# Kernel optimization log

Hardware: AMD Instinct MI355X
Metric: run time of the kernel (lower is better)

The kernel has to match this reference:

```python
import math
import jax, jax.numpy as jnp
import numpy as np

D_MODEL = 1024
N_HEAD = 16
HEAD_DIM = D_MODEL // N_HEAD
ATTN_MULT = 1.0
# standparam=False (muP): scaling = head_dim**-1 * sqrt(attn_mult)
SCALING = (1.0 / HEAD_DIM) * math.sqrt(ATTN_MULT)
EPS = 1e-5


def layernorm(x, w, b):
    mu = jnp.mean(x, axis=-1, keepdims=True)
    var = jnp.mean(jnp.square(x - mu), axis=-1, keepdims=True)
    return (x - mu) * jax.lax.rsqrt(var + EPS) * w + b


def setup_inputs() -> dict:
    key = jax.random.key(0)
    ks = jax.random.split(key, 6)
    L, N, E = 2048, 2, D_MODEL
    std = 0.02
    return {
        "x": jax.random.normal(ks[0], (L, N, E), jnp.float32),
        "ln1_w": jnp.ones((E,), jnp.float32),
        "ln1_b": jnp.zeros((E,), jnp.float32),
        "in_proj_w": jax.random.normal(ks[1], (3 * E, E), jnp.float32) * std,
        "in_proj_b": jnp.zeros((3 * E,), jnp.float32),
        "out_w": jax.random.normal(ks[2], (E, E), jnp.float32) * std,
        "out_b": jnp.zeros((E,), jnp.float32),
        "ln2_w": jnp.ones((E,), jnp.float32),
        "ln2_b": jnp.zeros((E,), jnp.float32),
        "fc_w": jax.random.normal(ks[3], (4 * E, E), jnp.float32) * std,
        "fc_b": jnp.zeros((4 * E,), jnp.float32),
        "proj_w": jax.random.normal(ks[4], (E, 4 * E), jnp.float32) * std,
        "proj_b": jnp.zeros((E,), jnp.float32),
    }


def block(x, ln1_w, ln1_b, in_proj_w, in_proj_b, out_w, out_b,
          ln2_w, ln2_b, fc_w, fc_b, proj_w, proj_b):
    L, N, E = x.shape
    H, D = N_HEAD, HEAD_DIM
    # --- self-attention on ln_1(x), seq-first layout (L, N, E) ---
    y = layernorm(x, ln1_w, ln1_b)
    qkv = jnp.einsum('lne,fe->lnf', y, in_proj_w) + in_proj_b  # (L, N, 3E)
    q, k, v = jnp.split(qkv, 3, axis=-1)
    q = q * SCALING
    # (L, N, E) -> (N, H, L, D)
    def to_heads(t):
        return t.reshape(L, N, H, D).transpose(1, 2, 0, 3)
    q, k, v = to_heads(q), to_heads(k), to_heads(v)
    scores = jnp.einsum('nhld,nhsd->nhls', q, k)           # (N, H, L, L)
    w = jax.nn.softmax(scores, axis=-1)
    o = jnp.einsum('nhls,nhsd->nhld', w, v)                # (N, H, L, D)
    o = o.transpose(2, 0, 1, 3).reshape(L, N, E)
    attn_out = jnp.einsum('lne,fe->lnf', o, out_w) + out_b
    x = x + attn_out
    # --- MLP on ln_2(x): fc -> GELU -> proj ---
    z = layernorm(x, ln2_w, ln2_b)
    h = jax.nn.gelu(jnp.einsum('lne,fe->lnf', z, fc_w) + fc_b, approximate=False)
    m = jnp.einsum('lnf,ef->lne', h, proj_w) + proj_b
    return x + m


def reference(x, ln1_w, ln1_b, in_proj_w, in_proj_b, out_w, out_b,
              ln2_w, ln2_b, fc_w, fc_b, proj_w, proj_b):
    return block(x, ln1_w, ln1_b, in_proj_w, in_proj_b, out_w, out_b,
                 ln2_w, ln2_b, fc_w, fc_b, proj_w, proj_b)
```

## Files before the change

kernel.cpp:

```cpp
#include <hip/hip_runtime.h>
#include <hip/hip_bf16.h>

typedef unsigned short u16;
typedef float v4f __attribute__((ext_vector_type(4)));
typedef __bf16 v8bf __attribute__((ext_vector_type(8)));
typedef unsigned short v4u __attribute__((ext_vector_type(4)));
typedef unsigned short v8u __attribute__((ext_vector_type(8)));

#define EMB 1024
#define TOK 4096
#define LSEQ 2048
#define NBATCH 2
#define SCALING 0.015625f
#define LN_EPS 1e-5f

template <int V> struct ic { static constexpr int v = V; };

__device__ __forceinline__ float bf2f(u16 u) {
  unsigned int i = ((unsigned int)u) << 16;
  return __builtin_bit_cast(float, i);
}
__device__ __forceinline__ u16 f2bf(float f) {
  __hip_bfloat16 h = __float2bfloat16(f);
  return __builtin_bit_cast(u16, h);
}
__device__ __forceinline__ v8bf load8(const u16* p) {
  return *reinterpret_cast<const v8bf*>(p);
}
__device__ __forceinline__ v4f mfma16(v8bf a, v8bf b, v4f c) {
  return __builtin_amdgcn_mfma_f32_16x16x32_bf16(a, b, c, 0, 0, 0);
}
__device__ __forceinline__ void gload16(const u16* g, u16* l) {
  __builtin_amdgcn_global_load_lds(
      (const __attribute__((address_space(1))) void*)g,
      (__attribute__((address_space(3))) void*)l, 16, 0, 0);
}
template <int N>
__device__ __forceinline__ void waitcnt_vm() {
  if constexpr (N == 0) asm volatile("s_waitcnt vmcnt(0)" ::: "memory");
  else if constexpr (N == 2) asm volatile("s_waitcnt vmcnt(2)" ::: "memory");
  else if constexpr (N == 3) asm volatile("s_waitcnt vmcnt(3)" ::: "memory");
  else if constexpr (N == 4) asm volatile("s_waitcnt vmcnt(4)" ::: "memory");
  else if constexpr (N == 6) asm volatile("s_waitcnt vmcnt(6)" ::: "memory");
  else if constexpr (N == 8) asm volatile("s_waitcnt vmcnt(8)" ::: "memory");
}
__device__ __forceinline__ float gelu_fast(float v) {
  float u = v * (0.7978845608f + 0.0356774081f * v * v);
  return v / (1.0f + __expf(-2.0f * u));
}

__global__ __launch_bounds__(256) void cvt_kernel(
    const float* __restrict__ in, u16* __restrict__ out) {
  size_t i = ((size_t)blockIdx.x * 256 + threadIdx.x) * 8;
  v4f a = *reinterpret_cast<const v4f*>(in + i);
  v4f b = *reinterpret_cast<const v4f*>(in + i + 4);
  v8u r;
#pragma unroll
  for (int j = 0; j < 4; j++) { r[j] = f2bf(a[j]); r[4 + j] = f2bf(b[j]); }
  *reinterpret_cast<v8u*>(out + i) = r;
}

__global__ __launch_bounds__(256) void addred_kernel(
    float* __restrict__ out, const u16* __restrict__ p0) {
  size_t i = ((size_t)blockIdx.x * 256 + threadIdx.x) * 8;
  v4f a0 = *reinterpret_cast<const v4f*>(out + i);
  v4f a1 = *reinterpret_cast<const v4f*>(out + i + 4);
  v8u pp = *reinterpret_cast<const v8u*>(p0 + i);
#pragma unroll
  for (int j = 0; j < 4; j++) {
    a0[j] += bf2f(pp[j]);
    a1[j] += bf2f(pp[4 + j]);
  }
  *reinterpret_cast<v4f*>(out + i) = a0;
  *reinterpret_cast<v4f*>(out + i + 4) = a1;
}

template <int MODE>
__global__ __launch_bounds__(256) void ln_kernel(
    const void* __restrict__ xin, const float* __restrict__ w,
    const float* __restrict__ b, u16* __restrict__ y) {
  int t = blockIdx.x, tid = threadIdx.x;
  float v[4];
  if (MODE == 0) {
    v4u raw = *reinterpret_cast<const v4u*>((const u16*)xin + (size_t)t * EMB + tid * 4);
#pragma unroll
    for (int j = 0; j < 4; j++) v[j] = bf2f(raw[j]);
  } else {
    v4f raw = *reinterpret_cast<const v4f*>((const float*)xin + (size_t)t * EMB + tid * 4);
#pragma unroll
    for (int j = 0; j < 4; j++) v[j] = raw[j];
  }
  float s = v[0] + v[1] + v[2] + v[3];
  float ss = v[0] * v[0] + v[1] * v[1] + v[2] * v[2] + v[3] * v[3];
#pragma unroll
  for (int off = 32; off >= 1; off >>= 1) {
    s += __shfl_xor(s, off);
    ss += __shfl_xor(ss, off);
  }
  __shared__ float sm[4], sq[4];
  if ((tid & 63) == 0) { sm[tid >> 6] = s; sq[tid >> 6] = ss; }
  __syncthreads();
  s = sm[0] + sm[1] + sm[2] + sm[3];
  ss = sq[0] + sq[1] + sq[2] + sq[3];
  float mu = s * (1.0f / EMB);
  float var = ss * (1.0f / EMB) - mu * mu;
  float rstd = rsqrtf(var + LN_EPS);
  v4f wv = *reinterpret_cast<const v4f*>(w + tid * 4);
  v4f bv = *reinterpret_cast<const v4f*>(b + tid * 4);
  v4u out;
#pragma unroll
  for (int j = 0; j < 4; j++) out[j] = f2bf((v[j] - mu) * rstd * wv[j] + bv[j]);
  *reinterpret_cast<v4u*>(y + (size_t)t * EMB + tid * 4) = out;
}

template <int BM, int BN>
__global__ __launch_bounds__(256) void gemm_db_kernel(
    const u16* __restrict__ A, const u16* __restrict__ W,
    const float* __restrict__ bias, int K, int Nout, int mode,
    u16* __restrict__ out_bf, float* __restrict__ out_f,
    const float* __restrict__ res_f32, const u16* __restrict__ res_bf) {
  constexpr int NJ = BM * BN / 4096;
  constexpr int CWV = 4 / (BM / 64);
  __shared__ alignas(16) u16 lA[2][BM * 32];
  __shared__ alignas(16) u16 lB[2][BN * 32];

  int tid = threadIdx.x;
  int lane = tid & 63, wid = tid >> 6;
  int quad = lane >> 4, l16 = lane & 15;
  int row0 = blockIdx.x * BM;
  int col0 = blockIdx.y * BN;
  int rw = (wid / CWV) * 64;
  int cw = (wid % CWV) * (BN / CWV);

  v4f zero = {0.f, 0.f, 0.f, 0.f};
  v4f acc[4][NJ];
#pragma unroll
  for (int i = 0; i < 4; i++)
#pragma unroll
    for (int j = 0; j < NJ; j++) acc[i][j] = zero;

  int wbase8 = (tid & 192) * 8;

  auto stage = [&](int buf, int k0) {
    const u16* Ab = A + (size_t)row0 * K + k0;
    const u16* Wb = W + (size_t)col0 * K + k0;
#pragma unroll
    for (int n = 0; n < BM / 64; n++) {
      int slot = n * 256 + tid;
      int seg = slot / BM, r = slot & (BM - 1);
      gload16(Ab + (size_t)r * K + seg * 8, &lA[buf][n * 2048 + wbase8]);
    }
#pragma unroll
    for (int n = 0; n < BN / 64; n++) {
      int slot = n * 256 + tid;
      int seg = slot / BN, r = slot & (BN - 1);
      gload16(Wb + (size_t)r * K + seg * 8, &lB[buf][n * 2048 + wbase8]);
    }
  };

  stage(0, 0);
  int buf = 0;
  for (int k0 = 0; k0 < K; k0 += 32) {
    __syncthreads();
    if (k0 + 32 < K) stage(buf ^ 1, k0 + 32);

    v8bf af[4], bfr[NJ];
#pragma unroll
    for (int i = 0; i < 4; i++)
      af[i] = load8(&lA[buf][(quad * BM + rw + i * 16 + l16) * 8]);
#pragma unroll
    for (int j = 0; j < NJ; j++)
      bfr[j] = load8(&lB[buf][(quad * BN + cw + j * 16 + l16) * 8]);
#pragma unroll
    for (int i = 0; i < 4; i++)
#pragma unroll
      for (int j = 0; j < NJ; j++)
        acc[i][j] = mfma16(af[i], bfr[j], acc[i][j]);
    buf ^= 1;
  }

#pragma unroll
  for (int i = 0; i < 4; i++) {
    int rbase = row0 + rw + i * 16 + quad * 4;
#pragma unroll
    for (int j = 0; j < NJ; j++) {
      int c = col0 + cw + j * 16 + l16;
      float bv = bias[c];
#pragma unroll
      for (int r = 0; r < 4; r++) {
        int tok = rbase + r;
        float v = acc[i][j][r] + bv;
        size_t idx = (size_t)tok * Nout + c;
        if (mode == 1) {
          out_bf[idx] = f2bf(res_f32[idx] + v);
        } else if (mode == 3) {
          out_f[idx] = bf2f(res_bf[idx]) + v;
        }
      }
    }
  }
}

template <int BM, int BN>
__global__ __launch_bounds__(512, 2) void gemm8_kernel(
    const u16* __restrict__ A, const u16* __restrict__ W,
    const float* __restrict__ bias, int K, int Nout, int mode,
    u16* __restrict__ out_bf, float* __restrict__ out_f,
    const u16* __restrict__ res_bf) {
  static_assert(BM == 256 && (BN == 128 || BN == 256), "geometry");
  constexpr int NJF = BN / 128;
  constexpr int LB = BN / 128;
  constexpr int H = BN / 8;
  __shared__ alignas(16) u16 lA[2][2][8192];
  __shared__ alignas(16) u16 lB[2][2][BN * 32];

  int tid = threadIdx.x;
  int lane = tid & 63, wid = tid >> 6;
  int quad = lane >> 4, l16 = lane & 15;
  int rwh = wid >> 2;
  int cwq = wid & 3;
  int row0 = blockIdx.x * BM, col0 = blockIdx.y * BN;

  int kbeg = 0, kend = K;
  if (mode == 5) { int h = K >> 1; kbeg = blockIdx.z * h; kend = kbeg + h; }
  int nt = (kend - kbeg) >> 6;

  v4f zero = {0.f, 0.f, 0.f, 0.f};
  v4f acc[8][2 * NJF];
#pragma unroll
  for (int i = 0; i < 8; i++)
#pragma unroll
    for (int j = 0; j < 2 * NJF; j++) acc[i][j] = zero;

  int wslot = tid & 448;

  auto stA = [&](int buf, int g, int kt) {
    int koff = kbeg + kt * 64;
#pragma unroll
    for (int n = 0; n < 2; n++) {
      int p = n * 512 + tid;
      int ri = p >> 3, sp = p & 7;
      int row = ((ri >> 6) << 7) | (g << 6) | (ri & 63);
      int sl = sp ^ (ri & 7);
      gload16(A + (size_t)(row0 + row) * K + koff + sl * 8,
              &lA[buf][g][(n * 512 + wslot) * 8]);
    }
  };
  auto stB = [&](int buf, int g, int kt) {
    int koff = kbeg + kt * 64;
#pragma unroll
    for (int n = 0; n < LB; n++) {
      int p = n * 512 + tid;
      int ci = p >> 3, sp = p & 7;
      int col = (ci / H) * (2 * H) + g * H + (ci % H);
      int sl = sp ^ (ci & 7);
      gload16(W + (size_t)(col0 + col) * K + koff + sl * 8,
              &lB[buf][g][(n * 512 + wslot) * 8]);
    }
  };

  auto rdA = [&](v8bf (&af)[4][2], int buf, int g) {
#pragma unroll
    for (int i = 0; i < 4; i++) {
      int ri = (rwh << 6) + i * 16 + l16;
      int rs = ri * 8, rx = ri & 7;
#pragma unroll
      for (int kk = 0; kk < 2; kk++)
        af[i][kk] = load8(&lA[buf][g][(rs + ((kk * 4 + quad) ^ rx)) * 8]);
    }
  };
  auto rdB = [&](v8bf (&bf)[NJF][2], int buf, int g) {
#pragma unroll
    for (int j = 0; j < NJF; j++) {
      int ci = cwq * H + j * 16 + l16;
      int rs = ci * 8, rx = ci & 7;
#pragma unroll
      for (int kk = 0; kk < 2; kk++)
        bf[j][kk] = load8(&lB[buf][g][(rs + ((kk * 4 + quad) ^ rx)) * 8]);
    }
  };
  auto mm = [&](auto QA, auto QB, v8bf (&af)[4][2], v8bf (&bf)[NJF][2]) {
    constexpr int qa = decltype(QA)::v, qb = decltype(QB)::v;
#pragma unroll
    for (int i = 0; i < 4; i++)
#pragma unroll
      for (int j = 0; j < NJF; j++)
#pragma unroll
        for (int kk = 0; kk < 2; kk++)
          acc[qa * 4 + i][qb * NJF + j] =
              mfma16(af[i][kk], bf[j][kk], acc[qa * 4 + i][qb * NJF + j]);
  };

  v8bf af[4][2], b0[NJF][2], b1[NJF][2];

  stA(0, 0, 0); stB(0, 0, 0); stB(0, 1, 0); stA(0, 1, 0);
  waitcnt_vm<2 + LB>();
  __builtin_amdgcn_s_barrier();

  for (int t = 0; t < nt - 1; ++t) {
    int buf = t & 1, nb = buf ^ 1;
    rdA(af, buf, 0); rdB(b0, buf, 0);
    stA(nb, 0, t + 1);
    __builtin_amdgcn_s_barrier();
    __builtin_amdgcn_s_setprio(1);
    mm(ic<0>{}, ic<0>{}, af, b0);
    __builtin_amdgcn_s_setprio(0);
    waitcnt_vm<4>();
    __builtin_amdgcn_s_barrier();
    rdB(b1, buf, 1);
    stB(nb, 0, t + 1);
    __builtin_amdgcn_s_barrier();
    __builtin_amdgcn_s_setprio(1);
    mm(ic<0>{}, ic<1>{}, af, b1);
    __builtin_amdgcn_s_setprio(0);
    waitcnt_vm<2 + LB>();
    __builtin_amdgcn_s_barrier();
    rdA(af, buf, 1);
    stB(nb, 1, t + 1);
    __builtin_amdgcn_s_barrier();
    __builtin_amdgcn_s_setprio(1);
    mm(ic<1>{}, ic<1>{}, af, b1);
    __builtin_amdgcn_s_setprio(0);
    __builtin_amdgcn_s_barrier();
    stA(nb, 1, t + 1);
    __builtin_amdgcn_s_barrier();
    __builtin_amdgcn_s_setprio(1);
    mm(ic<1>{}, ic<0>{}, af, b0);
    __builtin_amdgcn_s_setprio(0);
    waitcnt_vm<2 + LB>();
    __builtin_amdgcn_s_barrier();
  }
  waitcnt_vm<0>();
  __builtin_amdgcn_s_barrier();
  {
    int buf = (nt - 1) & 1;
    rdA(af, buf, 0); rdB(b0, buf, 0); rdB(b1, buf, 1);
    mm(ic<0>{}, ic<0>{}, af, b0);
    mm(ic<0>{}, ic<1>{}, af, b1);
    rdA(af, buf, 1);
    mm(ic<1>{}, ic<1>{}, af, b1);
    mm(ic<1>{}, ic<0>{}, af, b0);
  }

  int rw = rwh << 7;
  int cw = cwq * (BN / 4);
#pragma unroll
  for (int i = 0; i < 8; i++) {
    int rbase = row0 + rw + i * 16 + quad * 4;
#pragma unroll
    for (int j = 0; j < 2 * NJF; j++) {
      int c = col0 + cw + j * 16 + l16;
      float bv = bias[c];
#pragma unroll
      for (int r = 0; r < 4; r++) {
        int tok = rbase + r;
        float raw = acc[i][j][r];
        float v = raw + bv;
        if (mode == 4) {
          int region = c >> 10;
          int cc = c & 1023;
          int hh = cc >> 6, dd = cc & 63;
          int l = tok >> 1, nn = tok & 1;
          size_t hb = (size_t)(nn * 16 + hh);
          if (region == 0) {
            out_bf[(hb * LSEQ + l) * 64 + dd] = f2bf(v * SCALING);
          } else if (region == 1) {
            out_bf[4194304 + (hb * LSEQ + l) * 64 + dd] = f2bf(v);
          } else {
            out_bf[8388608 + (hb * 64 + dd) * LSEQ + l] = f2bf(v);
          }
        } else {
          size_t idx = (size_t)tok * Nout + c;
          if (mode == 2) {
            out_bf[idx] = f2bf(gelu_fast(v));
          } else {
            if (blockIdx.z == 0) {
              out_bf[idx] = f2bf(raw);
            } else {
              out_f[idx] = v + bf2f(res_bf[idx]);
            }
          }
        }
      }
    }
  }
}

__global__ __launch_bounds__(512) void flash_kernel(
    const u16* __restrict__ qb, const u16* __restrict__ kb,
    const u16* __restrict__ vtb, u16* __restrict__ o) {
  int tid = threadIdx.x;
  int lane = tid & 63, wid = tid >> 6;
  int quad = lane >> 4, l16 = lane & 15;
  int qt = blockIdx.x;
  int nh = blockIdx.y;
  int n = nh >> 4, h = nh & 15;

  __shared__ alignas(16) u16 lK[4096];
  __shared__ alignas(16) u16 lV[4096];
  __shared__ alignas(16) u16 pl[128][72];

  const u16* khead = kb + (size_t)nh * (LSEQ * 64);
  const u16* vhead = vtb + (size_t)nh * (64 * LSEQ);

  v4f zero = {0.f, 0.f, 0.f, 0.f};
  v4f acc_o[4];
  float lsum[4];
#pragma unroll
  for (int r = 0; r < 4; r++) lsum[r] = 0.f;
#pragma unroll
  for (int jd = 0; jd < 4; jd++) acc_o[jd] = zero;

  v8bf qf[2];
  {
    int lq = qt * 128 + wid * 16 + l16;
#pragma unroll
    for (int kk = 0; kk < 2; kk++)
      qf[kk] = load8(qb + ((size_t)nh * LSEQ + lq) * 64 + kk * 32 + quad * 8);
  }

  int swl = l16 & 7;
  int srow = tid >> 3;
  int sseg0 = tid & 7;
  int lbase = (tid & 448) * 8;

  for (int s0 = 0; s0 < LSEQ; s0 += 64) {
    {
      int seg = sseg0 ^ (srow & 7);
      gload16(khead + (size_t)(s0 + srow) * 64 + seg * 8, &lK[lbase]);
      gload16(vhead + (size_t)srow * LSEQ + s0 + seg * 8, &lV[lbase]);
    }
    __syncthreads();

    v4f sacc[4];
#pragma unroll
    for (int j = 0; j < 4; j++) sacc[j] = zero;
#pragma unroll
    for (int kk = 0; kk < 2; kk++) {
      v8bf kf[4];
#pragma unroll
      for (int j = 0; j < 4; j++) {
        int rl = j * 16 + l16;
        kf[j] = load8(&lK[((rl << 3) + (((kk << 2) + quad) ^ swl)) << 3]);
      }
#pragma unroll
      for (int j = 0; j < 4; j++)
        sacc[j] = mfma16(qf[kk], kf[j], sacc[j]);
    }

#pragma unroll
    for (int r = 0; r < 4; r++) {
      float ps = 0.f;
#pragma unroll
      for (int j = 0; j < 4; j++) {
        float p = __expf(fminf(sacc[j][r], 60.f));
        ps += p;
        pl[wid * 16 + quad * 4 + r][j * 16 + l16] = f2bf(p);
      }
      lsum[r] += ps;
    }

#pragma unroll
    for (int kk = 0; kk < 2; kk++) {
      v8bf pf, vf[4];
      pf = load8(&pl[wid * 16 + l16][kk * 32 + quad * 8]);
#pragma unroll
      for (int jd = 0; jd < 4; jd++) {
        int dl = jd * 16 + l16;
        vf[jd] = load8(&lV[((dl << 3) + (((kk << 2) + quad) ^ swl)) << 3]);
      }
#pragma unroll
      for (int jd = 0; jd < 4; jd++)
        acc_o[jd] = mfma16(pf, vf[jd], acc_o[jd]);
    }
    __syncthreads();
  }

#pragma unroll
  for (int r = 0; r < 4; r++) {
    float s = lsum[r];
#pragma unroll
    for (int off = 1; off < 16; off <<= 1) s += __shfl_xor(s, off);
    float inv = 1.0f / s;
    int lq = qt * 128 + wid * 16 + quad * 4 + r;
    size_t t = (size_t)lq * NBATCH + n;
#pragma unroll
    for (int jd = 0; jd < 4; jd++)
      o[t * EMB + h * 64 + jd * 16 + l16] = f2bf(acc_o[jd][r] * inv);
  }
}

extern "C" void kernel_launch(void* const* d_in, const int* in_sizes, int n_in,
                              void* d_out, int out_size, void* d_ws,
                              size_t ws_size, hipStream_t stream) {
  const float* x = (const float*)d_in[0];
  const float* ln1_w = (const float*)d_in[1];
  const float* ln1_b = (const float*)d_in[2];
  const float* in_proj_w = (const float*)d_in[3];
  const float* in_proj_b = (const float*)d_in[4];
  const float* out_w = (const float*)d_in[5];
  const float* out_b = (const float*)d_in[6];
  const float* ln2_w = (const float*)d_in[7];
  const float* ln2_b = (const float*)d_in[8];
  const float* fc_w = (const float*)d_in[9];
  const float* fc_b = (const float*)d_in[10];
  const float* proj_w = (const float*)d_in[11];
  const float* proj_b = (const float*)d_in[12];
  float* out = (float*)d_out;

  char* ws = (char*)d_ws;
  u16* wbuf = (u16*)(ws + 0);
  u16* y = (u16*)(ws + 8388608);
  u16* qkvh = (u16*)(ws + 16777216);
  u16* o = (u16*)(ws + 8388608);
  u16* hbuf = (u16*)(ws + 8388608);
  u16* x2 = (u16*)(ws + 41943040);
  u16* z = (u16*)(ws + 50331648);

  u16* qb = qkvh;
  u16* kb = qkvh + 4194304;
  u16* vtb = qkvh + 8388608;

  ln_kernel<1><<<TOK, 256, 0, stream>>>((const void*)x, ln1_w, ln1_b, y);
  cvt_kernel<<<1536, 256, 0, stream>>>(in_proj_w, wbuf);
  gemm8_kernel<256, 256><<<dim3(16, 12), 512, 0, stream>>>(
      y, wbuf, in_proj_b, EMB, 3 * EMB, 4, qkvh, nullptr, nullptr);
  flash_kernel<<<dim3(16, 32), 512, 0, stream>>>(qb, kb, vtb, o);
  cvt_kernel<<<512, 256, 0, stream>>>(out_w, wbuf);
  gemm_db_kernel<64, 128><<<dim3(64, 8), 256, 0, stream>>>(
      o, wbuf, out_b, EMB, EMB, 1, x2, nullptr, x, nullptr);
  ln_kernel<0><<<TOK, 256, 0, stream>>>((const void*)x2, ln2_w, ln2_b, z);
  cvt_kernel<<<2048, 256, 0, stream>>>(fc_w, wbuf);
  gemm8_kernel<256, 256><<<dim3(16, 16), 512, 0, stream>>>(
      z, wbuf, fc_b, EMB, 4 * EMB, 2, hbuf, nullptr, nullptr);
  cvt_kernel<<<2048, 256, 0, stream>>>(proj_w, wbuf);
  gemm8_kernel<256, 128><<<dim3(16, 8, 2), 512, 0, stream>>>(
      hbuf, wbuf, proj_b, 4 * EMB, EMB, 5, z, out, x2);
  addred_kernel<<<2048, 256, 0, stream>>>(out, z);
}
```

Before: 419.1 us.

## Swizzle GEMM LDS tiles and double-buffer K/V tiles in flash attention

The GEMM staging now stores A and W tiles in a row-major, XOR-swizzled LDS layout, and the fragment loads use the matching addresses, to reduce LDS bank conflicts. The flash-attention kernel gets double-buffered K and V LDS tiles: the next tile is prefetched with direct global-to-LDS loads and selective vmcnt waits while the current tile is computed, hiding global load latency. This doubles K/V LDS use, which could lower occupancy. It also relies on raw s_barrier placement being correct with respect to the waits.

```diff
diff --git a/kernel.cpp b/kernel.cpp
--- a/kernel.cpp
+++ b/kernel.cpp
@@ -146,15 +146,17 @@
     const u16* Wb = W + (size_t)col0 * K + k0;
 #pragma unroll
     for (int n = 0; n < BM / 64; n++) {
-      int slot = n * 256 + tid;
-      int seg = slot / BM, r = slot & (BM - 1);
-      gload16(Ab + (size_t)r * K + seg * 8, &lA[buf][n * 2048 + wbase8]);
+      int p = n * 256 + tid;
+      int r = p >> 2, sp = p & 3;
+      int sl = sp ^ ((r >> 1) & 3);
+      gload16(Ab + (size_t)r * K + sl * 8, &lA[buf][n * 2048 + wbase8]);
     }
 #pragma unroll
     for (int n = 0; n < BN / 64; n++) {
-      int slot = n * 256 + tid;
-      int seg = slot / BN, r = slot & (BN - 1);
-      gload16(Wb + (size_t)r * K + seg * 8, &lB[buf][n * 2048 + wbase8]);
+      int p = n * 256 + tid;
+      int r = p >> 2, sp = p & 3;
+      int sl = sp ^ ((r >> 1) & 3);
+      gload16(Wb + (size_t)r * K + sl * 8, &lB[buf][n * 2048 + wbase8]);
     }
   };
 
@@ -166,11 +168,15 @@
 
     v8bf af[4], bfr[NJ];
 #pragma unroll
-    for (int i = 0; i < 4; i++)
-      af[i] = load8(&lA[buf][(quad * BM + rw + i * 16 + l16) * 8]);
-#pragma unroll
-    for (int j = 0; j < NJ; j++)
-      bfr[j] = load8(&lB[buf][(quad * BN + cw + j * 16 + l16) * 8]);
+    for (int i = 0; i < 4; i++) {
+      int ra = rw + i * 16 + l16;
+      af[i] = load8(&lA[buf][((ra << 2) + (quad ^ ((ra >> 1) & 3))) << 3]);
+    }
+#pragma unroll
+    for (int j = 0; j < NJ; j++) {
+      int rb = cw + j * 16 + l16;
+      bfr[j] = load8(&lB[buf][((rb << 2) + (quad ^ ((rb >> 1) & 3))) << 3]);
+    }
 #pragma unroll
     for (int i = 0; i < 4; i++)
 #pragma unroll
@@ -396,8 +402,8 @@
   int nh = blockIdx.y;
   int n = nh >> 4, h = nh & 15;
 
-  __shared__ alignas(16) u16 lK[4096];
-  __shared__ alignas(16) u16 lV[4096];
+  __shared__ alignas(16) u16 lK[2][4096];
+  __shared__ alignas(16) u16 lV[2][4096];
   __shared__ alignas(16) u16 pl[128][72];
 
   const u16* khead = kb + (size_t)nh * (LSEQ * 64);
@@ -423,14 +429,23 @@
   int srow = tid >> 3;
   int sseg0 = tid & 7;
   int lbase = (tid & 448) * 8;
-
+  int sseg = sseg0 ^ (srow & 7);
+
+  gload16(khead + (size_t)srow * 64 + sseg * 8, &lK[0][lbase]);
+  gload16(vhead + (size_t)srow * LSEQ + 0 + sseg * 8, &lV[0][lbase]);
+
+  int buf = 0;
   for (int s0 = 0; s0 < LSEQ; s0 += 64) {
-    {
-      int seg = sseg0 ^ (srow & 7);
-      gload16(khead + (size_t)(s0 + srow) * 64 + seg * 8, &lK[lbase]);
-      gload16(vhead + (size_t)srow * LSEQ + s0 + seg * 8, &lV[lbase]);
-    }
-    __syncthreads();
+    if (s0 + 64 < LSEQ) {
+      gload16(khead + (size_t)(s0 + 64 + srow) * 64 + sseg * 8,
+              &lK[buf ^ 1][lbase]);
+      gload16(vhead + (size_t)srow * LSEQ + (s0 + 64) + sseg * 8,
+              &lV[buf ^ 1][lbase]);
+      waitcnt_vm<2>();
+    } else {
+      waitcnt_vm<0>();
+    }
+    __builtin_amdgcn_s_barrier();
 
     v4f sacc[4];
 #pragma unroll
@@ -441,7 +456,7 @@
 #pragma unroll
       for (int j = 0; j < 4; j++) {
         int rl = j * 16 + l16;
-        kf[j] = load8(&lK[((rl << 3) + (((kk << 2) + quad) ^ swl)) << 3]);
+        kf[j] = load8(&lK[buf][((rl << 3) + (((kk << 2) + quad) ^ swl)) << 3]);
       }
 #pragma unroll
       for (int j = 0; j < 4; j++)
@@ -467,13 +482,14 @@
 #pragma unroll
       for (int jd = 0; jd < 4; jd++) {
         int dl = jd * 16 + l16;
-        vf[jd] = load8(&lV[((dl << 3) + (((kk << 2) + quad) ^ swl)) << 3]);
+        vf[jd] = load8(&lV[buf][((dl << 3) + (((kk << 2) + quad) ^ swl)) << 3]);
       }
 #pragma unroll
       for (int jd = 0; jd < 4; jd++)
         acc_o[jd] = mfma16(pf, vf[jd], acc_o[jd]);
     }
-    __syncthreads();
+    __builtin_amdgcn_s_barrier();
+    buf ^= 1;
   }
 
 #pragma unroll
```

Measured after the change: 406.5 us. 1.03x faster.
